# Kernel tuning notes

Hardware: AMD Instinct MI355X
Metric: run time of the kernel (lower is better)

Reference implementation:

```python
import jax, jax.numpy as jnp
import numpy as np

H = 128  # GRU hidden size


def _conv(x, w, b, stride):
    # x: NCHW, w: OIHW, VALID padding (torch Conv2d default padding=0)
    y = jax.lax.conv_general_dilated(x, w, (stride, stride), 'VALID',
                                     dimension_numbers=('NCHW', 'OIHW', 'NCHW'))
    return y + b[None, :, None, None]


def setup_inputs() -> dict:
    key = jax.random.key(0)
    ks = jax.random.split(key, 16)
    T, B, A = 128, 32, 6
    x = jax.random.uniform(ks[0], (T * B, 1, 84, 84), jnp.float32) * 255.0
    done = (jax.random.uniform(ks[1], (T * B,)) < 0.1).astype(jnp.float32)
    gru_state = jnp.zeros((1, B, H), jnp.float32)
    s = 0.05
    params = dict(
        conv1_w=jax.random.normal(ks[2], (32, 1, 8, 8)) * s,
        conv1_b=jnp.zeros((32,)),
        conv2_w=jax.random.normal(ks[3], (64, 32, 4, 4)) * s,
        conv2_b=jnp.zeros((64,)),
        conv3_w=jax.random.normal(ks[4], (64, 64, 3, 3)) * s,
        conv3_b=jnp.zeros((64,)),
        fc_w=jax.random.normal(ks[5], (512, 64 * 7 * 7)) * 0.02,
        fc_b=jnp.zeros((512,)),
        w_ih=jax.random.normal(ks[6], (3 * H, 512)) * 0.04,
        w_hh=jax.random.normal(ks[7], (3 * H, H)) * 0.08,
        b_ih=jnp.zeros((3 * H,)),
        b_hh=jnp.zeros((3 * H,)),
        actor_w=jax.random.normal(ks[8], (A, H)) * 0.01,
        actor_b=jnp.zeros((A,)),
        critic_w=jax.random.normal(ks[9], (1, H)) * 0.09,
        critic_b=jnp.zeros((1,)),
    )
    return dict(x=x, done=done, gru_state=gru_state, **params)


def reference(x, done, gru_state,
              conv1_w, conv1_b, conv2_w, conv2_b, conv3_w, conv3_b,
              fc_w, fc_b, w_ih, w_hh, b_ih, b_hh,
              actor_w, actor_b, critic_w, critic_b):
    # CNN encoder on x/255
    h = jax.nn.relu(_conv(x / 255.0, conv1_w, conv1_b, 4))  # [N,32,20,20]
    h = jax.nn.relu(_conv(h, conv2_w, conv2_b, 2))          # [N,64,9,9]
    h = jax.nn.relu(_conv(h, conv3_w, conv3_b, 1))          # [N,64,7,7]
    feat = jax.nn.relu(h.reshape(h.shape[0], -1) @ fc_w.T + fc_b)  # [N,512]

    B = gru_state.shape[1]
    feat = feat.reshape(-1, B, feat.shape[-1])  # [T,B,512]
    d = done.reshape(-1, B)                     # [T,B]

    # hoist input-to-gate projection out of the scan
    gx = jnp.einsum('tbi,gi->tbg', feat, w_ih) + b_ih  # [T,B,3H]

    def step(hprev, inp):
        gxt, dt = inp
        hprev = (1.0 - dt)[:, None] * hprev  # done-reset mask
        gh = hprev @ w_hh.T + b_hh           # [B,3H]
        r = jax.nn.sigmoid(gxt[:, :H] + gh[:, :H])
        z = jax.nn.sigmoid(gxt[:, H:2 * H] + gh[:, H:2 * H])
        n = jnp.tanh(gxt[:, 2 * H:] + r * gh[:, 2 * H:])
        hnew = (1.0 - z) * n + z * hprev
        return hnew, hnew

    h_final, hs = jax.lax.scan(step, gru_state[0], (gx, d))
    hidden = hs.reshape(-1, H)  # [T*B,H]

    logits = hidden @ actor_w.T + actor_b   # [N,A]
    value = hidden @ critic_w.T + critic_b  # [N,1]
    return logits, value, h_final[None]
```

## Files before the change

### kernel.cpp

```cpp
#include <hip/hip_runtime.h>
#include <hip/hip_bf16.h>
#include <stdint.h>

#define DI __device__ __forceinline__

typedef __bf16 bf16x8 __attribute__((ext_vector_type(8)));
typedef __bf16 bf16x4 __attribute__((ext_vector_type(4)));
typedef float f32x16 __attribute__((ext_vector_type(16)));
typedef float f32x2 __attribute__((ext_vector_type(2)));

DI float bf2f(unsigned short u){ return __uint_as_float(((unsigned int)u)<<16); }
DI unsigned short f2bf(float f){
  unsigned int x = __float_as_uint(f);
  x += 0x7fffu + ((x>>16)&1u);
  return (unsigned short)(x>>16);
}
DI float sigmoidf_(float x){ return 1.0f/(1.0f + __expf(-x)); }
DI float tanhf_(float x){ return 2.0f/(1.0f + __expf(-2.0f*x)) - 1.0f; }

DI void gld_lds16(const void* g, void* l){
  __builtin_amdgcn_global_load_lds((const __attribute__((address_space(1))) void*)g,
                                   (__attribute__((address_space(3))) void*)l, 16, 0, 0);
}
DI f32x16 mfma32(bf16x8 a, bf16x8 b, f32x16 c){
  return __builtin_amdgcn_mfma_f32_32x32x16_bf16(a, b, c, 0, 0, 0);
}

__global__ __launch_bounds__(256) void k_prep_w1(const float* __restrict__ w1, unsigned short* __restrict__ o){
  int idx = blockIdx.x*256 + threadIdx.x;
  int j=idx&7, l=(idx>>3)&63, kk=idx>>9;
  int oc=l&31, kg=kk*16+((l>>5)<<3)+j;
  o[idx] = f2bf(w1[oc*64 + kg] * (1.0f/255.0f));
}
__global__ __launch_bounds__(256) void k_prep_w2(const float* __restrict__ w2, unsigned short* __restrict__ o){
  int idx = blockIdx.x*256 + threadIdx.x;
  int j=idx&7, l=(idx>>3)&63, nt=(idx>>9)&1, kh=(idx>>10)&1, s=idx>>11;
  int oc=nt*32+(l&31), ic=kh*16+(l>>5)*8+j, ky=s>>2, kx=s&3;
  o[idx] = f2bf(w2[((oc*32+ic)*4+ky)*4+kx]);
}
__global__ __launch_bounds__(256) void k_prep_w3(const float* __restrict__ w3, unsigned short* __restrict__ o){
  int idx = blockIdx.x*256 + threadIdx.x;
  int j=idx&7, l=(idx>>3)&63, nt=(idx>>9)&1, kh=(idx>>10)&3, s=idx>>12;
  int oc=nt*32+(l&31), ic=kh*16+(l>>5)*8+j, ky=s/3, kx=s-ky*3;
  o[idx] = f2bf(w3[((oc*64+ic)*3+ky)*3+kx]);
}
__global__ __launch_bounds__(512) void k_prep_fc(const float* __restrict__ fcw, unsigned short* __restrict__ o){
  int tid=threadIdx.x, ks=blockIdx.x, nt=blockIdx.y;
  int j=tid&7, l=tid>>3;
  int n=nt*32+(l&31), k=ks*16+(l>>5)*8+j;
  int c=k&63, pos=k>>6;
  float wv = fcw[(size_t)n*3136 + c*49 + pos];
  unsigned short hi = f2bf(wv);
  int idx = (nt*196+ks)*512 + tid;
  o[idx] = hi;
  o[1605632 + idx] = f2bf(wv - bf2f(hi));
}
__global__ __launch_bounds__(512) void k_prep_gx(const float* __restrict__ wih, unsigned short* __restrict__ o){
  int tid=threadIdx.x, ks=blockIdx.x, nt=blockIdx.y;
  int j=tid&7, l=tid>>3;
  int n=nt*32+(l&31), k=ks*16+(l>>5)*8+j;
  float wv = wih[(size_t)n*512 + k];
  unsigned short hi = f2bf(wv);
  int idx = (nt*32+ks)*512 + tid;
  o[idx] = hi;
  o[196608 + idx] = f2bf(wv - bf2f(hi));
}

__global__ __launch_bounds__(256) void k_conv1(const float* __restrict__ x,
    const unsigned short* __restrict__ w1p, const float* __restrict__ b,
    unsigned short* __restrict__ a1, int nbase)
{
  __shared__ __align__(16) char imgs[4*14784];
  const int tid=threadIdx.x, l=tid&63, w=tid>>6;
  const int nloc = blockIdx.x*4 + w;
  char* myimg = imgs + w*14784;
  const float* xp = x + (size_t)(nbase+nloc)*7056;

  for (int it=0; it<28; ++it){
    int idx4 = l + it*64;
    if (idx4 < 1764){
      float4 v = *(const float4*)(xp + idx4*4);
      int row = idx4/21, rem = idx4 - row*21;
      ushort4 u; u.x=f2bf(v.x); u.y=f2bf(v.y); u.z=f2bf(v.z); u.w=f2bf(v.w);
      *(ushort4*)(myimg + row*176 + rem*8) = u;
    }
  }

  bf16x8 wb[4];
  #pragma unroll
  for (int kk=0;kk<4;kk++) wb[kk] = *(const bf16x8*)(w1p + (kk*64 + l)*8);
  const float bias = b[l&31];
  asm volatile("s_waitcnt lgkmcnt(0)" ::: "memory");

  const int kyh = (l>>5);
  unsigned short* obase = a1 + (size_t)nloc*12800;
  for (int mt=0; mt<13; ++mt){
    int p = mt*32 + (l&31);
    p = min(p, 399);
    const int oy = p/20, ox = p - oy*20;
    const int rbyte = oy*4*176 + ox*8;
    f32x16 acc = {};
    #pragma unroll
    for (int kk=0;kk<4;kk++){
      const int a = rbyte + (kk*2 + kyh)*176;
      bf16x8 af;
      *(bf16x4*)&af       = *(const bf16x4*)(myimg + a);
      *((bf16x4*)&af + 1) = *(const bf16x4*)(myimg + a + 8);
      acc = mfma32(af, wb[kk], acc);
    }
    const int oc = l&31;
    #pragma unroll
    for (int rg=0;rg<16;rg++){
      int row = (rg&3) + 8*(rg>>2) + 4*kyh;
      int pos = mt*32 + row;
      if (pos < 400)
        obase[pos*32 + oc] = f2bf(fmaxf(acc[rg] + bias, 0.f));
    }
  }
}

__global__ __launch_bounds__(256) void k_conv2(const unsigned short* __restrict__ a1,
    const unsigned short* __restrict__ w2p, const float* __restrict__ b2,
    unsigned short* __restrict__ a2, int nbase)
{
  extern __shared__ __align__(16) char smem[];
  const int tid=threadIdx.x, l=tid&63, w=tid>>6;
  const int nloc = blockIdx.x*4 + w;
  char* myimg = smem + w*25600;
  const char* gimg = (const char*)(a1 + (size_t)nloc*12800);
  #pragma unroll
  for (int i=0;i<25;i++){
    int o = i*1024 + l*16;
    int q = o ^ (((o>>7)&7)<<4);
    gld_lds16(gimg + q, myimg + i*1024);
  }
  __syncthreads();
  int rbase[3];
  #pragma unroll
  for (int mt=0;mt<3;mt++){
    int r = mt*32 + (l&31);
    int oy=r/9, ox=r-oy*9;
    rbase[mt] = 40*oy + 2*ox;
  }
  const int grp16 = (l>>5)*16;
  f32x16 acc[3][2] = {};
  #pragma unroll
  for (int ky=0;ky<4;ky++){
    #pragma unroll
    for (int kx=0;kx<4;kx++){
      const int s = ky*4+kx;
      #pragma unroll
      for (int kh=0;kh<2;kh++){
        bf16x8 b0 = *(const bf16x8*)(w2p + (((s*2+kh)*2+0)*64 + l)*8);
        bf16x8 b1 = *(const bf16x8*)(w2p + (((s*2+kh)*2+1)*64 + l)*8);
        #pragma unroll
        for (int mt=0;mt<3;mt++){
          int ip = rbase[mt] + ky*20 + kx;
          ip = min(ip, 399);
          int byte = (ip*64 + kh*32 + grp16) ^ (((ip>>1)&7)<<4);
          bf16x8 af = *(const bf16x8*)(myimg + byte);
          acc[mt][0] = mfma32(af, b0, acc[mt][0]);
          acc[mt][1] = mfma32(af, b1, acc[mt][1]);
        }
      }
    }
  }
  const float bias0 = b2[l&31], bias1 = b2[32+(l&31)];
  unsigned short* ob = (unsigned short*)myimg;
  #pragma unroll
  for (int mt=0;mt<3;mt++){
    #pragma unroll
    for (int rg=0;rg<16;rg++){
      int r = mt*32 + (rg&3) + 8*(rg>>2) + 4*(l>>5);
      ob[r*64 + (l&31)]      = f2bf(fmaxf(acc[mt][0][rg]+bias0,0.f));
      ob[r*64 + 32 + (l&31)] = f2bf(fmaxf(acc[mt][1][rg]+bias1,0.f));
    }
  }
  asm volatile("s_waitcnt lgkmcnt(0)" ::: "memory");
  const uint4* s4 = (const uint4*)ob;
  uint4* d4 = (uint4*)(a2 + (size_t)(nbase+nloc)*5184);
  #pragma unroll
  for (int i=0;i<11;i++){
    int c = i*64 + l;
    if (c < 648) d4[c] = s4[c];
  }
}

__global__ __launch_bounds__(256) void k_conv3(const unsigned short* __restrict__ a2,
    const unsigned short* __restrict__ w3p, const float* __restrict__ b3,
    unsigned short* __restrict__ a3)
{
  __shared__ __align__(16) char smem3[4*11264];
  const int tid=threadIdx.x, l=tid&63, w=tid>>6;
  const int n = blockIdx.x*4 + w;
  char* myimg = smem3 + w*11264;
  const char* gimg = (const char*)(a2 + (size_t)n*5184);
  #pragma unroll
  for (int i=0;i<11;i++){
    int c = i*64 + l;
    int cc = min(c, 647);
    int o = cc*16;
    int q = o ^ (((o>>7)&7)<<4);
    gld_lds16(gimg + q, myimg + i*1024);
  }
  __syncthreads();
  int base[2];
  #pragma unroll
  for (int mt=0;mt<2;mt++){
    int r = mt*32 + (l&31);
    int oy=r/7, ox=r-oy*7;
    base[mt] = oy*9 + ox;
  }
  const int grp16 = (l>>5)*16;
  f32x16 acc[2][2] = {};
  #pragma unroll
  for (int ky=0;ky<3;ky++){
    #pragma unroll
    for (int kx=0;kx<3;kx++){
      const int s = ky*3+kx;
      #pragma unroll
      for (int kh=0;kh<4;kh++){
        bf16x8 b0 = *(const bf16x8*)(w3p + (((s*4+kh)*2+0)*64 + l)*8);
        bf16x8 b1 = *(const bf16x8*)(w3p + (((s*4+kh)*2+1)*64 + l)*8);
        #pragma unroll
        for (int mt=0;mt<2;mt++){
          int ip = min(base[mt] + ky*9 + kx, 80);
          int byte = (ip*128 + kh*32 + grp16) ^ ((ip&7)<<4);
          bf16x8 af = *(const bf16x8*)(myimg + byte);
          acc[mt][0] = mfma32(af, b0, acc[mt][0]);
          acc[mt][1] = mfma32(af, b1, acc[mt][1]);
        }
      }
    }
  }
  const float bias0 = b3[l&31], bias1 = b3[32+(l&31)];
  unsigned short* ob = (unsigned short*)myimg;
  #pragma unroll
  for (int mt=0;mt<2;mt++){
    #pragma unroll
    for (int rg=0;rg<16;rg++){
      int r = mt*32 + (rg&3) + 8*(rg>>2) + 4*(l>>5);
      if (r < 49){
        ob[r*64 + (l&31)]      = f2bf(fmaxf(acc[mt][0][rg]+bias0,0.f));
        ob[r*64 + 32 + (l&31)] = f2bf(fmaxf(acc[mt][1][rg]+bias1,0.f));
      }
    }
  }
  asm volatile("s_waitcnt lgkmcnt(0)" ::: "memory");
  const uint4* s4 = (const uint4*)ob;
  uint4* d4 = (uint4*)(a3 + (size_t)n*3136);
  #pragma unroll
  for (int i=0;i<7;i++){
    int c = i*64 + l;
    if (c < 392) d4[c] = s4[c];
  }
}

template<bool RELU, bool OBF16>
__global__ __launch_bounds__(256) void k_gemm(const unsigned short* __restrict__ A, int K,
    const unsigned short* __restrict__ Wp, int loOff, const float* __restrict__ bias,
    void* __restrict__ out, int N)
{
  __shared__ __align__(16) char ab[2][8192];
  const int tid=threadIdx.x, l=tid&63, w=tid>>6;
  const int m0=blockIdx.y*128, n0=blockIdx.x*64;
  const int KS=K>>4, T=K>>5;
  const int mh=w&1, ntl=w>>1;
  const int ntg = blockIdx.x*2 + ntl;
  const char* Ab = (const char*)A;

  f32x16 acc[2] = {};
  bf16x8 bh0, bh1, bl0, bl1, nh0, nh1, nl0, nl1;

  #pragma unroll
  for (int i=0;i<2;i++){
    int o = (w*2+i)*1024 + l*16;
    int q = o ^ (((o>>7)&7)<<4);
    int row = q>>6, kc=(q>>4)&3;
    gld_lds16(Ab + ((size_t)(m0+row)*K)*2 + kc*16, ab[0] + (w*2+i)*1024);
  }
  {
    const unsigned short* p0 = Wp + ((size_t)(ntg*KS)*64 + l)*8;
    bh0 = *(const bf16x8*)(p0);
    bh1 = *(const bf16x8*)(p0 + 512);
    bl0 = *(const bf16x8*)(p0 + loOff);
    bl1 = *(const bf16x8*)(p0 + loOff + 512);
  }
  __syncthreads();

  for (int t=0;t<T;t++){
    const int cb = t&1;
    if (t+1 < T){
      #pragma unroll
      for (int i=0;i<2;i++){
        int o = (w*2+i)*1024 + l*16;
        int q = o ^ (((o>>7)&7)<<4);
        int row = q>>6, kc=(q>>4)&3;
        gld_lds16(Ab + ((size_t)(m0+row)*K + (t+1)*32)*2 + kc*16, ab[cb^1] + (w*2+i)*1024);
      }
      const unsigned short* pn = Wp + ((size_t)(ntg*KS + (t+1)*2)*64 + l)*8;
      nh0 = *(const bf16x8*)(pn);
      nh1 = *(const bf16x8*)(pn + 512);
      nl0 = *(const bf16x8*)(pn + loOff);
      nl1 = *(const bf16x8*)(pn + loOff + 512);
    }
    #pragma unroll
    for (int mt=0;mt<2;mt++){
      int r = mh*64 + mt*32 + (l&31);
      int b0 = (r*64 + (l>>5)*16) ^ (((r>>1)&7)<<4);
      bf16x8 a0 = *(const bf16x8*)(ab[cb] + b0);
      bf16x8 a1 = *(const bf16x8*)(ab[cb] + (b0^32));
      acc[mt] = mfma32(a0, bh0, acc[mt]);
      acc[mt] = mfma32(a1, bh1, acc[mt]);
      acc[mt] = mfma32(a0, bl0, acc[mt]);
      acc[mt] = mfma32(a1, bl1, acc[mt]);
    }
    __syncthreads();
    bh0=nh0; bh1=nh1; bl0=nl0; bl1=nl1;
  }

  const int col = n0 + ntl*32 + (l&31);
  const float bv = bias[col];
  #pragma unroll
  for (int mt=0;mt<2;mt++){
    #pragma unroll
    for (int rg=0;rg<16;rg++){
      int r = m0 + mh*64 + mt*32 + (rg&3) + 8*(rg>>2) + 4*(l>>5);
      float v = acc[mt][rg] + bv;
      if (RELU) v = fmaxf(v, 0.f);
      if (OBF16) ((unsigned short*)out)[(size_t)r*N + col] = f2bf(v);
      else       ((float*)out)[(size_t)r*N + col] = v;
    }
  }
}

__global__ __launch_bounds__(512) void k_gru(const float* __restrict__ gx,
    const float* __restrict__ done, const float* __restrict__ h0,
    const float* __restrict__ whh, const float* __restrict__ bhh,
    float* __restrict__ hid, float* __restrict__ hfin)
{
  __shared__ __align__(16) float hs[2][128];
  const int b = blockIdx.x, tid = threadIdx.x;
  const int u = tid>>2, sub = tid&3;
  f32x2 wr[16], wz[16], wn[16];
  const float* wru = whh + (size_t)u*128 + sub*32;
  const float* wzu = whh + (size_t)(u+128)*128 + sub*32;
  const float* wnu = whh + (size_t)(u+256)*128 + sub*32;
  #pragma unroll
  for (int q=0;q<8;q++){
    const int e = (q + sub*2)&7;
    float4 a = *(const float4*)(wru + e*4);
    float4 c = *(const float4*)(wzu + e*4);
    float4 d = *(const float4*)(wnu + e*4);
    wr[q*2] = f32x2{a.x,a.y}; wr[q*2+1] = f32x2{a.z,a.w};
    wz[q*2] = f32x2{c.x,c.y}; wz[q*2+1] = f32x2{c.z,c.w};
    wn[q*2] = f32x2{d.x,d.y}; wn[q*2+1] = f32x2{d.z,d.w};
  }
  const float br = bhh[u], bz = bhh[u+128], bn = bhh[u+256];
  if (tid<128) hs[0][tid] = h0[(size_t)b*128+tid];

  const float* g0 = gx + (size_t)b*384;
  float pg0 = g0[u], pg1 = g0[u+128], pg2 = g0[u+256];
  float pd  = done[b];
  __syncthreads();

  for (int t=0;t<128;t++){
    const int cur = t&1;
    const float gr=pg0, gz=pg1, gn=pg2, dn=pd;
    if (t+1 < 128){
      const float* gp = gx + ((size_t)(t+1)*32+b)*384;
      pg0=gp[u]; pg1=gp[u+128]; pg2=gp[u+256];
      pd = done[(t+1)*32+b];
    }
    const float hpv = hs[cur][u];
    const float* hb = &hs[cur][sub*32];
    f32x2 hv[16];
    #pragma unroll
    for (int q=0;q<8;q++){
      const int e = (q + sub*2)&7;
      float4 v = *(const float4*)(hb + e*4);
      hv[q*2]   = f32x2{v.x,v.y};
      hv[q*2+1] = f32x2{v.z,v.w};
    }
    f32x2 a2r = {0.f,0.f}, a2z = {0.f,0.f}, a2n = {0.f,0.f};
    #pragma unroll
    for (int i=0;i<16;i++){
      a2r += wr[i]*hv[i];
      a2z += wz[i]*hv[i];
      a2n += wn[i]*hv[i];
    }
    float ar=a2r[0]+a2r[1], az=a2z[0]+a2z[1], an=a2n[0]+a2n[1];
    ar += __shfl_xor(ar,1); ar += __shfl_xor(ar,2);
    az += __shfl_xor(az,1); az += __shfl_xor(az,2);
    an += __shfl_xor(an,1); an += __shfl_xor(an,2);
    if (sub==0){
      const float keep = 1.0f - dn;
      const float hp = keep*hpv;
      const float r  = sigmoidf_(gr + keep*ar + br);
      const float z  = sigmoidf_(gz + keep*az + bz);
      const float nn = tanhf_  (gn + r*(keep*an + bn));
      const float hn = (1.0f-z)*nn + z*hp;
      hs[cur^1][u] = hn;
      hid[((size_t)t*32+b)*128 + u] = hn;
    }
    asm volatile("s_waitcnt lgkmcnt(0)\n\ts_barrier" ::: "memory");
    __builtin_amdgcn_sched_barrier(0);
  }
  if (tid<128) hfin[(size_t)b*128+tid] = hs[0][tid];
}

__global__ __launch_bounds__(256) void k_heads(const float* __restrict__ hid,
    const float* __restrict__ aw, const float* __restrict__ ab,
    const float* __restrict__ cw, const float* __restrict__ cb,
    float* __restrict__ out)
{
  __shared__ __align__(16) float wsm[7*128];
  __shared__ float bb[7];
  const int tid = threadIdx.x;
  for (int i=tid;i<896;i+=256) wsm[i] = (i<768) ? aw[i] : cw[i-768];
  if (tid<7) bb[tid] = (tid<6) ? ab[tid] : cb[0];
  __syncthreads();
  const int idx = blockIdx.x*256 + tid;
  const int n = idx/7, a = idx - n*7;
  const float4* hp = (const float4*)(hid + (size_t)n*128);
  const float4* wp = (const float4*)(&wsm[a*128]);
  float s = bb[a];
  #pragma unroll
  for (int q=0;q<32;q++){
    const float4 h4=hp[q], w4=wp[q];
    s += h4.x*w4.x + h4.y*w4.y + h4.z*w4.z + h4.w*w4.w;
  }
  if (a<6) out[(size_t)n*6+a]=s; else out[24576+n]=s;
}

extern "C" void kernel_launch(void* const* d_in, const int* in_sizes, int n_in,
                              void* d_out, int out_size, void* d_ws, size_t ws_size,
                              hipStream_t stream)
{
  const float* x    = (const float*)d_in[0];
  const float* done = (const float*)d_in[1];
  const float* h0   = (const float*)d_in[2];
  const float* c1w  = (const float*)d_in[3];
  const float* c1b  = (const float*)d_in[4];
  const float* c2w  = (const float*)d_in[5];
  const float* c2b  = (const float*)d_in[6];
  const float* c3w  = (const float*)d_in[7];
  const float* c3b  = (const float*)d_in[8];
  const float* fcw  = (const float*)d_in[9];
  const float* fcb  = (const float*)d_in[10];
  const float* wih  = (const float*)d_in[11];
  const float* whh  = (const float*)d_in[12];
  const float* bih  = (const float*)d_in[13];
  const float* bhh  = (const float*)d_in[14];
  const float* aw   = (const float*)d_in[15];
  const float* ab   = (const float*)d_in[16];
  const float* cw   = (const float*)d_in[17];
  const float* cb   = (const float*)d_in[18];
  float* out = (float*)d_out;
  char* ws = (char*)d_ws;

  unsigned short* W1P  = (unsigned short*)(ws);
  unsigned short* W2P  = (unsigned short*)(ws + 4096);
  unsigned short* W3P  = (unsigned short*)(ws + 69632);
  unsigned short* FCWP = (unsigned short*)(ws + 143360);
  unsigned short* GXWP = (unsigned short*)(ws + 6565888);
  unsigned short* A1   = (unsigned short*)(ws + 7352320);
  unsigned short* A2   = (unsigned short*)(ws + 59781120);
  unsigned short* A3   = (unsigned short*)(ws + 7352320);
  unsigned short* FEAT = (unsigned short*)(ws + 33042432);
  float* GX   = (float*)(ws + 37236736);
  float* HID  = (float*)(ws + 43528192);

  static bool attr_set = false;
  if (!attr_set) {
    (void)hipFuncSetAttribute((const void*)k_conv2, hipFuncAttributeMaxDynamicSharedMemorySize, 102400);
    attr_set = true;
  }

  k_prep_w1<<<8, 256, 0, stream>>>(c1w, W1P);
  k_prep_w2<<<128, 256, 0, stream>>>(c2w, W2P);
  k_prep_w3<<<144, 256, 0, stream>>>(c3w, W3P);
  k_prep_fc<<<dim3(196,16), 512, 0, stream>>>(fcw, FCWP);
  k_prep_gx<<<dim3(32,12), 512, 0, stream>>>(wih, GXWP);

  for (int pass=0; pass<2; pass++){
    k_conv1<<<512, 256, 0, stream>>>(x, W1P, c1b, A1, pass*2048);
    k_conv2<<<512, 256, 102400, stream>>>(A1, W2P, c2b, A2, pass*2048);
  }
  k_conv3<<<1024, 256, 0, stream>>>(A2, W3P, c3b, A3);
  k_gemm<true, true ><<<dim3(8,32), 256, 0, stream>>>(A3, 3136, FCWP, 1605632, fcb, (void*)FEAT, 512);
  k_gemm<false,false><<<dim3(6,32), 256, 0, stream>>>(FEAT, 512, GXWP, 196608, bih, (void*)GX, 384);
  k_gru<<<32, 512, 0, stream>>>(GX, done, h0, whh, bhh, HID, out + 28672);
  k_heads<<<112, 256, 0, stream>>>(HID, aw, ab, cw, cb, out);
}
```

Baseline: 361.2 us.

## Merge weight prep kernels, drop fc lo-split MFMAs, halve GRU block size

Combines the five weight-preparation kernels into a single launch dispatched by block range, removing several launch overheads. The fc GEMM now uses only the bf16 high part of the weights, which halves its MFMA work and weight loads but lowers accuracy. The GRU kernel moves to 256 threads with 2 lanes per hidden unit, which doubles the per-thread register weights and removes one shuffle stage per reduction. The wider per-thread weight arrays add register pressure in the GRU.

```diff
diff --git a/kernel.cpp b/kernel.cpp
--- a/kernel.cpp
+++ b/kernel.cpp
@@ -26,44 +26,51 @@
   return __builtin_amdgcn_mfma_f32_32x32x16_bf16(a, b, c, 0, 0, 0);
 }
 
-__global__ __launch_bounds__(256) void k_prep_w1(const float* __restrict__ w1, unsigned short* __restrict__ o){
-  int idx = blockIdx.x*256 + threadIdx.x;
-  int j=idx&7, l=(idx>>3)&63, kk=idx>>9;
-  int oc=l&31, kg=kk*16+((l>>5)<<3)+j;
-  o[idx] = f2bf(w1[oc*64 + kg] * (1.0f/255.0f));
-}
-__global__ __launch_bounds__(256) void k_prep_w2(const float* __restrict__ w2, unsigned short* __restrict__ o){
-  int idx = blockIdx.x*256 + threadIdx.x;
-  int j=idx&7, l=(idx>>3)&63, nt=(idx>>9)&1, kh=(idx>>10)&1, s=idx>>11;
-  int oc=nt*32+(l&31), ic=kh*16+(l>>5)*8+j, ky=s>>2, kx=s&3;
-  o[idx] = f2bf(w2[((oc*32+ic)*4+ky)*4+kx]);
-}
-__global__ __launch_bounds__(256) void k_prep_w3(const float* __restrict__ w3, unsigned short* __restrict__ o){
-  int idx = blockIdx.x*256 + threadIdx.x;
-  int j=idx&7, l=(idx>>3)&63, nt=(idx>>9)&1, kh=(idx>>10)&3, s=idx>>12;
-  int oc=nt*32+(l&31), ic=kh*16+(l>>5)*8+j, ky=s/3, kx=s-ky*3;
-  o[idx] = f2bf(w3[((oc*64+ic)*3+ky)*3+kx]);
-}
-__global__ __launch_bounds__(512) void k_prep_fc(const float* __restrict__ fcw, unsigned short* __restrict__ o){
-  int tid=threadIdx.x, ks=blockIdx.x, nt=blockIdx.y;
-  int j=tid&7, l=tid>>3;
-  int n=nt*32+(l&31), k=ks*16+(l>>5)*8+j;
-  int c=k&63, pos=k>>6;
-  float wv = fcw[(size_t)n*3136 + c*49 + pos];
-  unsigned short hi = f2bf(wv);
-  int idx = (nt*196+ks)*512 + tid;
-  o[idx] = hi;
-  o[1605632 + idx] = f2bf(wv - bf2f(hi));
-}
-__global__ __launch_bounds__(512) void k_prep_gx(const float* __restrict__ wih, unsigned short* __restrict__ o){
-  int tid=threadIdx.x, ks=blockIdx.x, nt=blockIdx.y;
-  int j=tid&7, l=tid>>3;
-  int n=nt*32+(l&31), k=ks*16+(l>>5)*8+j;
-  float wv = wih[(size_t)n*512 + k];
-  unsigned short hi = f2bf(wv);
-  int idx = (nt*32+ks)*512 + tid;
-  o[idx] = hi;
-  o[196608 + idx] = f2bf(wv - bf2f(hi));
+__global__ __launch_bounds__(256) void k_prep_all(
+    const float* __restrict__ w1, const float* __restrict__ w2, const float* __restrict__ w3,
+    const float* __restrict__ fcw, const float* __restrict__ wih,
+    unsigned short* __restrict__ W1P, unsigned short* __restrict__ W2P,
+    unsigned short* __restrict__ W3P, unsigned short* __restrict__ FCWP,
+    unsigned short* __restrict__ GXWP)
+{
+  const int blk = blockIdx.x, tid = threadIdx.x;
+  if (blk < 8){
+    int idx = blk*256 + tid;
+    int j=idx&7, l=(idx>>3)&63, kk=idx>>9;
+    int oc=l&31, kg=kk*16+((l>>5)<<3)+j;
+    W1P[idx] = f2bf(w1[oc*64 + kg] * (1.0f/255.0f));
+  } else if (blk < 136){
+    int idx = (blk-8)*256 + tid;
+    int j=idx&7, l=(idx>>3)&63, nt=(idx>>9)&1, kh=(idx>>10)&1, s=idx>>11;
+    int oc=nt*32+(l&31), ic=kh*16+(l>>5)*8+j, ky=s>>2, kx=s&3;
+    W2P[idx] = f2bf(w2[((oc*32+ic)*4+ky)*4+kx]);
+  } else if (blk < 280){
+    int idx = (blk-136)*256 + tid;
+    int j=idx&7, l=(idx>>3)&63, nt=(idx>>9)&1, kh=(idx>>10)&3, s=idx>>12;
+    int oc=nt*32+(l&31), ic=kh*16+(l>>5)*8+j, ky=s/3, kx=s-ky*3;
+    W3P[idx] = f2bf(w3[((oc*64+ic)*3+ky)*3+kx]);
+  } else if (blk < 6552){
+    int i = (blk-280)*256 + tid;
+    int t2 = i&511, rest = i>>9;
+    int ks = rest%196, nt = rest/196;
+    int j=t2&7, l=t2>>3;
+    int n=nt*32+(l&31), k=ks*16+(l>>5)*8+j;
+    int c=k&63, pos=k>>6;
+    float wv = fcw[(size_t)n*3136 + c*49 + pos];
+    unsigned short hi = f2bf(wv);
+    FCWP[i] = hi;
+    FCWP[1605632 + i] = f2bf(wv - bf2f(hi));
+  } else {
+    int i = (blk-6552)*256 + tid;
+    int t2 = i&511, rest = i>>9;
+    int ks = rest&31, nt = rest>>5;
+    int j=t2&7, l=t2>>3;
+    int n=nt*32+(l&31), k=ks*16+(l>>5)*8+j;
+    float wv = wih[(size_t)n*512 + k];
+    unsigned short hi = f2bf(wv);
+    GXWP[i] = hi;
+    GXWP[196608 + i] = f2bf(wv - bf2f(hi));
+  }
 }
 
 __global__ __launch_bounds__(256) void k_conv1(const float* __restrict__ x,
@@ -256,7 +263,7 @@
   }
 }
 
-template<bool RELU, bool OBF16>
+template<bool RELU, bool OBF16, bool HILO>
 __global__ __launch_bounds__(256) void k_gemm(const unsigned short* __restrict__ A, int K,
     const unsigned short* __restrict__ Wp, int loOff, const float* __restrict__ bias,
     void* __restrict__ out, int N)
@@ -283,8 +290,10 @@
     const unsigned short* p0 = Wp + ((size_t)(ntg*KS)*64 + l)*8;
     bh0 = *(const bf16x8*)(p0);
     bh1 = *(const bf16x8*)(p0 + 512);
-    bl0 = *(const bf16x8*)(p0 + loOff);
-    bl1 = *(const bf16x8*)(p0 + loOff + 512);
+    if (HILO){
+      bl0 = *(const bf16x8*)(p0 + loOff);
+      bl1 = *(const bf16x8*)(p0 + loOff + 512);
+    }
   }
   __syncthreads();
 
@@ -301,8 +310,10 @@
       const unsigned short* pn = Wp + ((size_t)(ntg*KS + (t+1)*2)*64 + l)*8;
       nh0 = *(const bf16x8*)(pn);
       nh1 = *(const bf16x8*)(pn + 512);
-      nl0 = *(const bf16x8*)(pn + loOff);
-      nl1 = *(const bf16x8*)(pn + loOff + 512);
+      if (HILO){
+        nl0 = *(const bf16x8*)(pn + loOff);
+        nl1 = *(const bf16x8*)(pn + loOff + 512);
+      }
     }
     #pragma unroll
     for (int mt=0;mt<2;mt++){
@@ -312,11 +323,14 @@
       bf16x8 a1 = *(const bf16x8*)(ab[cb] + (b0^32));
       acc[mt] = mfma32(a0, bh0, acc[mt]);
       acc[mt] = mfma32(a1, bh1, acc[mt]);
-      acc[mt] = mfma32(a0, bl0, acc[mt]);
-      acc[mt] = mfma32(a1, bl1, acc[mt]);
+      if (HILO){
+        acc[mt] = mfma32(a0, bl0, acc[mt]);
+        acc[mt] = mfma32(a1, bl1, acc[mt]);
+      }
     }
     __syncthreads();
-    bh0=nh0; bh1=nh1; bl0=nl0; bl1=nl1;
+    bh0=nh0; bh1=nh1;
+    if (HILO){ bl0=nl0; bl1=nl1; }
   }
 
   const int col = n0 + ntl*32 + (l&31);
@@ -334,21 +348,21 @@
   }
 }
 
-__global__ __launch_bounds__(512) void k_gru(const float* __restrict__ gx,
+__global__ __launch_bounds__(256) void k_gru(const float* __restrict__ gx,
     const float* __restrict__ done, const float* __restrict__ h0,
     const float* __restrict__ whh, const float* __restrict__ bhh,
     float* __restrict__ hid, float* __restrict__ hfin)
 {
   __shared__ __align__(16) float hs[2][128];
   const int b = blockIdx.x, tid = threadIdx.x;
-  const int u = tid>>2, sub = tid&3;
-  f32x2 wr[16], wz[16], wn[16];
-  const float* wru = whh + (size_t)u*128 + sub*32;
-  const float* wzu = whh + (size_t)(u+128)*128 + sub*32;
-  const float* wnu = whh + (size_t)(u+256)*128 + sub*32;
-  #pragma unroll
-  for (int q=0;q<8;q++){
-    const int e = (q + sub*2)&7;
+  const int u = tid>>1, sub = tid&1;
+  f32x2 wr[32], wz[32], wn[32];
+  const float* wru = whh + (size_t)u*128 + sub*64;
+  const float* wzu = whh + (size_t)(u+128)*128 + sub*64;
+  const float* wnu = whh + (size_t)(u+256)*128 + sub*64;
+  #pragma unroll
+  for (int q=0;q<16;q++){
+    const int e = (q + sub*4)&15;
     float4 a = *(const float4*)(wru + e*4);
     float4 c = *(const float4*)(wzu + e*4);
     float4 d = *(const float4*)(wnu + e*4);
@@ -373,26 +387,26 @@
       pd = done[(t+1)*32+b];
     }
     const float hpv = hs[cur][u];
-    const float* hb = &hs[cur][sub*32];
-    f32x2 hv[16];
-    #pragma unroll
-    for (int q=0;q<8;q++){
-      const int e = (q + sub*2)&7;
+    const float* hb = &hs[cur][sub*64];
+    f32x2 hv[32];
+    #pragma unroll
+    for (int q=0;q<16;q++){
+      const int e = (q + sub*4)&15;
       float4 v = *(const float4*)(hb + e*4);
       hv[q*2]   = f32x2{v.x,v.y};
       hv[q*2+1] = f32x2{v.z,v.w};
     }
     f32x2 a2r = {0.f,0.f}, a2z = {0.f,0.f}, a2n = {0.f,0.f};
     #pragma unroll
-    for (int i=0;i<16;i++){
+    for (int i=0;i<32;i++){
       a2r += wr[i]*hv[i];
       a2z += wz[i]*hv[i];
       a2n += wn[i]*hv[i];
     }
     float ar=a2r[0]+a2r[1], az=a2z[0]+a2z[1], an=a2n[0]+a2n[1];
-    ar += __shfl_xor(ar,1); ar += __shfl_xor(ar,2);
-    az += __shfl_xor(az,1); az += __shfl_xor(az,2);
-    an += __shfl_xor(an,1); an += __shfl_xor(an,2);
+    ar += __shfl_xor(ar,1);
+    az += __shfl_xor(az,1);
+    an += __shfl_xor(an,1);
     if (sub==0){
       const float keep = 1.0f - dn;
       const float hp = keep*hpv;
@@ -477,19 +491,15 @@
     attr_set = true;
   }
 
-  k_prep_w1<<<8, 256, 0, stream>>>(c1w, W1P);
-  k_prep_w2<<<128, 256, 0, stream>>>(c2w, W2P);
-  k_prep_w3<<<144, 256, 0, stream>>>(c3w, W3P);
-  k_prep_fc<<<dim3(196,16), 512, 0, stream>>>(fcw, FCWP);
-  k_prep_gx<<<dim3(32,12), 512, 0, stream>>>(wih, GXWP);
+  k_prep_all<<<7320, 256, 0, stream>>>(c1w, c2w, c3w, fcw, wih, W1P, W2P, W3P, FCWP, GXWP);
 
   for (int pass=0; pass<2; pass++){
     k_conv1<<<512, 256, 0, stream>>>(x, W1P, c1b, A1, pass*2048);
     k_conv2<<<512, 256, 102400, stream>>>(A1, W2P, c2b, A2, pass*2048);
   }
   k_conv3<<<1024, 256, 0, stream>>>(A2, W3P, c3b, A3);
-  k_gemm<true, true ><<<dim3(8,32), 256, 0, stream>>>(A3, 3136, FCWP, 1605632, fcb, (void*)FEAT, 512);
-  k_gemm<false,false><<<dim3(6,32), 256, 0, stream>>>(FEAT, 512, GXWP, 196608, bih, (void*)GX, 384);
-  k_gru<<<32, 512, 0, stream>>>(GX, done, h0, whh, bhh, HID, out + 28672);
+  k_gemm<true, true, false><<<dim3(8,32), 256, 0, stream>>>(A3, 3136, FCWP, 0, fcb, (void*)FEAT, 512);
+  k_gemm<false,false,true ><<<dim3(6,32), 256, 0, stream>>>(FEAT, 512, GXWP, 196608, bih, (void*)GX, 384);
+  k_gru<<<32, 256, 0, stream>>>(GX, done, h0, whh, bhh, HID, out + 28672);
   k_heads<<<112, 256, 0, stream>>>(HID, aw, ab, cw, cb, out);
 }
```

Result: faster. 342.2 us (-5.3%).
